# Performance work log

Measured on AMD Instinct MI355X. Metric: run time of the kernel, lower is better.

The kernel has to match this reference:

```python
import jax, jax.numpy as jnp
import numpy as np

NEG_SLOPE = 0.2


def setup_inputs() -> dict:
    key = jax.random.key(0)
    ks = jax.random.split(key, 6)
    N, E, IN, H, D = 50000, 800000, 256, 4, 64
    x = jax.random.normal(ks[0], (N, IN), dtype=jnp.float32)
    edge_index = jax.random.randint(ks[1], (2, E), 0, N, dtype=jnp.int64)
    W = jax.random.normal(ks[2], (IN, H * D), dtype=jnp.float32) / np.sqrt(IN)
    att_src = jax.random.normal(ks[3], (H, D), dtype=jnp.float32) / np.sqrt(D)
    att_dst = jax.random.normal(ks[4], (H, D), dtype=jnp.float32) / np.sqrt(D)
    bias = jnp.zeros((H * D,), dtype=jnp.float32)
    return {"x": x, "edge_index": edge_index, "W": W,
            "att_src": att_src, "att_dst": att_dst, "bias": bias}


def reference(x, edge_index, W, att_src, att_dst, bias):
    N = x.shape[0]
    H, D = att_src.shape
    # add self-loops (PyG GATConv default add_self_loops=True)
    loops = jnp.arange(N, dtype=edge_index.dtype)
    src = jnp.concatenate([edge_index[0], loops])  # [E']
    dst = jnp.concatenate([edge_index[1], loops])  # [E']
    # per-head linear transform: [N, H, D]
    h = (x @ W).reshape(N, H, D)
    # per-node attention logits per head: [N, H]
    a_s = jnp.einsum('nhd,hd->nh', h, att_src)
    a_d = jnp.einsum('nhd,hd->nh', h, att_dst)
    # per-edge raw attention: [E', H]
    e = jax.nn.leaky_relu(a_s[src] + a_d[dst], NEG_SLOPE)
    # softmax over edges grouped by destination node (stable)
    m = jax.ops.segment_max(e, dst, num_segments=N)
    e = jnp.exp(e - m[dst])
    s = jax.ops.segment_sum(e, dst, num_segments=N)
    alpha = e / s[dst]  # every node has a self-loop -> s > 0
    # weighted scatter-aggregate: [N, H, D]
    out = jax.ops.segment_sum(alpha[:, :, None] * h[src], dst, num_segments=N)
    # concat heads + bias; dropout=0.0 -> identity
    return out.reshape(N, H * D) + bias
```

## Files before the change

### kernel.cpp

```cpp
#include <hip/hip_runtime.h>
#include <hip/hip_bf16.h>

#define NEG_SLOPE 0.2f
#define HPAD 264

typedef short short8 __attribute__((ext_vector_type(8)));
typedef float floatx4 __attribute__((ext_vector_type(4)));
typedef unsigned short ushort8v __attribute__((ext_vector_type(8)));
typedef unsigned short ushort4v __attribute__((ext_vector_type(4)));
typedef unsigned int uint4v __attribute__((ext_vector_type(4)));

__device__ __forceinline__ float bf2f_raw(unsigned short u) {
    union { float f; unsigned u; } c; c.u = ((unsigned)u) << 16; return c.f;
}
__device__ __forceinline__ float asf(unsigned u) {
    union { float f; unsigned u; } c; c.u = u; return c.f;
}
__device__ __forceinline__ unsigned short f2bf_raw(float f) {
    union { float f; unsigned u; } c; c.f = f;
    unsigned u = c.u;
    u += 0x7FFFu + ((u >> 16) & 1u);
    return (unsigned short)(u >> 16);
}
__device__ __forceinline__ float ldf(const void* p, size_t i, int f32) {
    return f32 ? ((const float*)p)[i] : bf2f_raw(((const unsigned short*)p)[i]);
}
__device__ __forceinline__ unsigned short ldbf(const void* p, size_t i, int f32) {
    return f32 ? f2bf_raw(((const float*)p)[i]) : ((const unsigned short*)p)[i];
}
__device__ __forceinline__ int clampN(long long v, int N) {
    if (v < 0) v = 0;
    if (v >= N) v = N - 1;
    return (int)v;
}
__device__ __forceinline__ float lrelu(float v) { return v > 0.f ? v : NEG_SLOPE * v; }

__global__ __launch_bounds__(256) void detect_kernel(
    const unsigned short* __restrict__ x, const unsigned short* __restrict__ W,
    const unsigned short* __restrict__ as_, const unsigned short* __restrict__ ad_,
    const unsigned* __restrict__ edge_w, int* __restrict__ flags, int edge_words)
{
    __shared__ float sm[256];
    __shared__ unsigned su[256];
    const int t = threadIdx.x;

    float mx = 0.f, mw = 0.f, ma = 0.f;
    for (int i = t; i < 4096; i += 256) {
        float v = fabsf(bf2f_raw(x[i]));
        mx = fmaxf(mx, (v == v && v < 3e38f) ? v : 1e9f);
    }
    for (int i = t; i < 4096; i += 256) {
        float v = fabsf(bf2f_raw(W[i]));
        mw = fmaxf(mw, (v == v && v < 3e38f) ? v : 1e9f);
    }
    {
        float v1 = fabsf(bf2f_raw(as_[t]));
        float v2 = fabsf(bf2f_raw(ad_[t]));
        v1 = (v1 == v1 && v1 < 3e38f) ? v1 : 1e9f;
        v2 = (v2 == v2 && v2 < 3e38f) ? v2 : 1e9f;
        ma = fmaxf(v1, v2);
    }
    unsigned ow = 0;
    {
        int i = 2 * t + 1;
        if (i < edge_words) ow = edge_w[i];
    }

    sm[t] = mx; __syncthreads();
    for (int s = 128; s; s >>= 1) { if (t < s) sm[t] = fmaxf(sm[t], sm[t + s]); __syncthreads(); }
    if (t == 0) flags[0] = sm[0] > 100.f;
    __syncthreads();

    sm[t] = mw; __syncthreads();
    for (int s = 128; s; s >>= 1) { if (t < s) sm[t] = fmaxf(sm[t], sm[t + s]); __syncthreads(); }
    if (t == 0) flags[1] = sm[0] > 100.f;
    __syncthreads();

    sm[t] = ma; __syncthreads();
    for (int s = 128; s; s >>= 1) { if (t < s) sm[t] = fmaxf(sm[t], sm[t + s]); __syncthreads(); }
    if (t == 0) flags[2] = sm[0] > 100.f;
    __syncthreads();

    su[t] = ow; __syncthreads();
    for (int s = 128; s; s >>= 1) { if (t < s) su[t] |= su[t + s]; __syncthreads(); }
    if (t == 0) flags[3] = (su[0] == 0u);
}

__global__ __launch_bounds__(256) void wt_kernel(
    const void* __restrict__ W, unsigned short* __restrict__ Wt,
    const int* __restrict__ flags, int* __restrict__ deg8, int* __restrict__ bsync, int N8)
{
    int i = blockIdx.x * 256 + threadIdx.x;
    #pragma unroll
    for (int j = 0; j < 7; ++j) {
        int z = i + j * 65536;
        if (z < N8) deg8[z] = 0;
    }
    if (i < 256) bsync[i] = 0;
    int j = i & 7;
    int l = (i >> 3) & 63;
    int ks = (i >> 9) & 7;
    int c = i >> 12;
    int k = ks * 32 + (l >> 4) * 8 + j;
    int n = c * 16 + (l & 15);
    Wt[i] = ldbf(W, (size_t)k * 256 + n, flags[1]);
}

__global__ __launch_bounds__(256) void count_kernel(
    const void* __restrict__ edge, int* __restrict__ deg8, int* __restrict__ rank,
    const int* __restrict__ flags, int E, int N)
{
    const int base = (blockIdx.x * 256 + threadIdx.x) * 4;
    if (base >= E) return;
    int* my = deg8 + (size_t)(blockIdx.x & 7) * N;
    const int cnt = (E - base < 4) ? (E - base) : 4;
    int d[4];
    if (flags[3]) {
        const long long* p = (const long long*)edge + E + base;
        #pragma unroll
        for (int k = 0; k < 4; ++k) d[k] = clampN((k < cnt) ? p[k] : 0, N);
    } else {
        const int* p = (const int*)edge + E + base;
        #pragma unroll
        for (int k = 0; k < 4; ++k) d[k] = clampN((k < cnt) ? (long long)p[k] : 0, N);
    }
    int r[4] = {0, 0, 0, 0};
    #pragma unroll
    for (int k = 0; k < 4; ++k)
        if (k < cnt) r[k] = atomicAdd(&my[d[k]], 1);
    #pragma unroll
    for (int k = 0; k < 4; ++k)
        if (k < cnt) rank[base + k] = r[k];
}

__global__ __launch_bounds__(512) void gemm_kernel(
    const void* __restrict__ x, const unsigned short* __restrict__ Wt,
    const void* __restrict__ att_src, const void* __restrict__ att_dst,
    unsigned short* __restrict__ h_out, float* __restrict__ a_s, float* __restrict__ a_d,
    const int* __restrict__ flags, int N, int ntiles, int gemm_blocks)
{
    __shared__ unsigned short sh_h[32][HPAD];
    __shared__ float sh_a[2][32][4];

    const int w = threadIdx.x >> 6;
    const int head = w >> 1;
    const int st = w & 1;
    const int l = threadIdx.x & 63;
    const int lane16 = l & 15;
    const int quad = l >> 4;
    const int xf = flags[0], af = flags[2];
    const int n0w = head * 64;

    float as_att[4], ad_att[4];
    #pragma unroll
    for (int nt = 0; nt < 4; ++nt) {
        as_att[nt] = ldf(att_src, n0w + nt * 16 + lane16, af);
        ad_att[nt] = ldf(att_dst, n0w + nt * 16 + lane16, af);
    }

    for (int tile = blockIdx.x; tile < ntiles; tile += gemm_blocks) {
        const int m0 = tile * 32;
        int r0 = m0 + st * 16 + lane16;
        if (r0 >= N) r0 = N - 1;

        floatx4 acc[4];
        #pragma unroll
        for (int nt = 0; nt < 4; ++nt) acc[nt] = (floatx4){0.f, 0.f, 0.f, 0.f};

        const unsigned short* wp0 = Wt + (((size_t)head * 32) * 64 + l) * 8;

        #pragma unroll
        for (int half = 0; half < 2; ++half) {
            short8 fa[4];
            if (!xf) {
                const char* b0 = (const char*)x + ((size_t)r0 * 256 + quad * 8) * 2 + half * 256;
                #pragma unroll
                for (int k4 = 0; k4 < 4; ++k4)
                    fa[k4] = *(const short8*)(b0 + k4 * 64);
            } else {
                const float* b0 = (const float*)x + (size_t)r0 * 256 + quad * 8 + half * 128;
                #pragma unroll
                for (int k4 = 0; k4 < 4; ++k4) {
                    #pragma unroll
                    for (int j = 0; j < 8; ++j)
                        fa[k4][j] = (short)f2bf_raw(b0[k4 * 32 + j]);
                }
            }

            #pragma unroll
            for (int k4 = 0; k4 < 4; ++k4) {
                const unsigned short* wp = wp0 + (size_t)(half * 4 + k4) * 512;
                #pragma unroll
                for (int nt = 0; nt < 4; ++nt) {
                    short8 fb = *(const short8*)(wp + nt * 4096);
                    acc[nt] = __builtin_amdgcn_mfma_f32_16x16x32_bf16(fa[k4], fb, acc[nt], 0, 0, 0);
                }
            }
        }

        __syncthreads();

        #pragma unroll
        for (int nt = 0; nt < 4; ++nt) {
            #pragma unroll
            for (int r = 0; r < 4; ++r) {
                sh_h[st * 16 + quad * 4 + r][n0w + nt * 16 + lane16] = f2bf_raw(acc[nt][r]);
            }
        }
        #pragma unroll
        for (int r = 0; r < 4; ++r) {
            float vs = acc[0][r] * as_att[0] + acc[1][r] * as_att[1]
                     + acc[2][r] * as_att[2] + acc[3][r] * as_att[3];
            float vd = acc[0][r] * ad_att[0] + acc[1][r] * ad_att[1]
                     + acc[2][r] * ad_att[2] + acc[3][r] * ad_att[3];
            vs += __shfl_xor(vs, 1); vs += __shfl_xor(vs, 2);
            vs += __shfl_xor(vs, 4); vs += __shfl_xor(vs, 8);
            vd += __shfl_xor(vd, 1); vd += __shfl_xor(vd, 2);
            vd += __shfl_xor(vd, 4); vd += __shfl_xor(vd, 8);
            if (lane16 == 0) {
                const int row = st * 16 + quad * 4 + r;
                sh_a[0][row][head] = vs;
                sh_a[1][row][head] = vd;
            }
        }

        __syncthreads();

        #pragma unroll
        for (int p = 0; p < 2; ++p) {
            const int c = p * 512 + threadIdx.x;
            const int row = c >> 5;
            const int ch = c & 31;
            if (m0 + row < N) {
                ushort8v v = *(const ushort8v*)&sh_h[row][ch * 8];
                *(ushort8v*)(h_out + (size_t)(m0 + row) * 256 + ch * 8) = v;
            }
        }
        {
            const int t = threadIdx.x;
            if (t < 32) {
                if (m0 + t < N)
                    *(floatx4*)&a_s[(size_t)(m0 + t) * 4] = *(const floatx4*)&sh_a[0][t][0];
            } else if (t >= 64 && t < 96) {
                const int r = t - 64;
                if (m0 + r < N)
                    *(floatx4*)&a_d[(size_t)(m0 + r) * 4] = *(const floatx4*)&sh_a[1][r][0];
            }
        }
    }
}

__global__ __launch_bounds__(256) void scan_fused_kernel(
    const int* __restrict__ deg8, int* __restrict__ deg,
    int* __restrict__ row_off, int* __restrict__ cursor8,
    int* __restrict__ bsum, int* __restrict__ bbase, int* __restrict__ bsync,
    int N, int nb)
{
    __shared__ int sh[256];
    __shared__ int is_last;
    __shared__ int sbase;
    const int b = blockIdx.x, t = threadIdx.x;
    const int base_i = b * 1024 + t * 4;
    int v[4], ts = 0;
    #pragma unroll
    for (int i = 0; i < 4; ++i) {
        int idx = base_i + i;
        int tot = 0;
        if (idx < N) {
            #pragma unroll
            for (int x = 0; x < 8; ++x) tot += deg8[(size_t)x * N + idx];
        }
        v[i] = tot;
        ts += tot;
    }
    sh[t] = ts; __syncthreads();
    for (int off = 1; off < 256; off <<= 1) {
        int add = (t >= off) ? sh[t - off] : 0;
        __syncthreads();
        sh[t] += add;
        __syncthreads();
    }
    if (t == 255) {
        __hip_atomic_store(&bsum[b], sh[255], __ATOMIC_RELEASE, __HIP_MEMORY_SCOPE_AGENT);
        int arrived = __hip_atomic_fetch_add(&bsync[0], 1, __ATOMIC_ACQ_REL, __HIP_MEMORY_SCOPE_AGENT);
        is_last = (arrived == nb - 1);
    }
    __syncthreads();
    if (is_last) {
        if (nb <= 64) {
            if (t < 64) {
                int val = (t < nb)
                    ? __hip_atomic_load(&bsum[t], __ATOMIC_ACQUIRE, __HIP_MEMORY_SCOPE_AGENT) : 0;
                int incl = val;
                #pragma unroll
                for (int off = 1; off < 64; off <<= 1) {
                    int u = __shfl_up(incl, off);
                    if (t >= off) incl += u;
                }
                if (t < nb)
                    __hip_atomic_store(&bbase[t], incl - val, __ATOMIC_RELEASE, __HIP_MEMORY_SCOPE_AGENT);
            }
        } else if (t == 0) {
            int run = 0;
            for (int i = 0; i < nb; ++i) {
                int s = __hip_atomic_load(&bsum[i], __ATOMIC_ACQUIRE, __HIP_MEMORY_SCOPE_AGENT);
                __hip_atomic_store(&bbase[i], run, __ATOMIC_RELEASE, __HIP_MEMORY_SCOPE_AGENT);
                run += s;
            }
        }
        __syncthreads();
        if (t == 0)
            __hip_atomic_store(&bsync[1], 1, __ATOMIC_RELEASE, __HIP_MEMORY_SCOPE_AGENT);
    }
    if (t == 0) {
        while (__hip_atomic_load(&bsync[1], __ATOMIC_ACQUIRE, __HIP_MEMORY_SCOPE_AGENT) == 0) {}
        sbase = __hip_atomic_load(&bbase[b], __ATOMIC_RELAXED, __HIP_MEMORY_SCOPE_AGENT);
    }
    __syncthreads();
    int run = sbase + sh[t] - ts;
    #pragma unroll
    for (int i = 0; i < 4; ++i) {
        int idx = base_i + i;
        if (idx < N) {
            row_off[idx] = run;
            deg[idx] = v[i];
            int c = run;
            #pragma unroll
            for (int x = 0; x < 8; ++x) {
                cursor8[(size_t)x * N + idx] = c;
                c += deg8[(size_t)x * N + idx];
            }
        }
        run += v[i];
    }
}

__global__ __launch_bounds__(256) void scatter_kernel(
    const void* __restrict__ edge, const int* __restrict__ cursor8,
    const int* __restrict__ rank, int* __restrict__ elist,
    const int* __restrict__ flags, int E, int N)
{
    const int base = (blockIdx.x * 256 + threadIdx.x) * 4;
    if (base >= E) return;
    const int* mybase = cursor8 + (size_t)(blockIdx.x & 7) * N;
    const int cnt = (E - base < 4) ? (E - base) : 4;
    int s[4], d[4];
    if (flags[3]) {
        const long long* ps = (const long long*)edge + base;
        const long long* pd = (const long long*)edge + E + base;
        #pragma unroll
        for (int k = 0; k < 4; ++k) {
            s[k] = clampN((k < cnt) ? ps[k] : 0, N);
            d[k] = clampN((k < cnt) ? pd[k] : 0, N);
        }
    } else {
        const int* ps = (const int*)edge + base;
        const int* pd = (const int*)edge + E + base;
        #pragma unroll
        for (int k = 0; k < 4; ++k) {
            s[k] = clampN((k < cnt) ? (long long)ps[k] : 0, N);
            d[k] = clampN((k < cnt) ? (long long)pd[k] : 0, N);
        }
    }
    #pragma unroll
    for (int k = 0; k < 4; ++k) {
        if (k < cnt) {
            int pos = mybase[d[k]] + rank[base + k];
            elist[pos] = s[k];
        }
    }
}

__global__ __launch_bounds__(256) void aggregate_kernel(
    const int* __restrict__ row_off, const int* __restrict__ deg,
    const int* __restrict__ elist,
    const float* __restrict__ a_s, const float* __restrict__ a_d,
    const unsigned short* __restrict__ h_ws,
    const void* __restrict__ bias, void* __restrict__ out,
    const int* __restrict__ flags, int N)
{
    const int n = blockIdx.x * 4 + (threadIdx.x >> 6);
    if (n >= N) return;
    const int lane = threadIdx.x & 63;
    const int q = lane >> 4;
    const int li = lane & 15;
    const int head = li >> 2;
    const int col0 = li * 16;

    const int dn = deg[n];
    const int row = row_off[n];
    const float adn = a_d[n * 4 + head];
    const float self_logit = lrelu(a_s[n * 4 + head] + adn);

    float acc[16];
    {
        const uint4v* hp = (const uint4v*)(h_ws + (size_t)n * 256 + col0);
        uint4v ha = hp[0], hb = hp[1];
        #pragma unroll
        for (int w = 0; w < 4; ++w) {
            acc[2 * w]         = (q == 0) ? asf(ha[w] << 16) : 0.f;
            acc[2 * w + 1]     = (q == 0) ? asf(ha[w] & 0xffff0000u) : 0.f;
            acc[8 + 2 * w]     = (q == 0) ? asf(hb[w] << 16) : 0.f;
            acc[8 + 2 * w + 1] = (q == 0) ? asf(hb[w] & 0xffff0000u) : 0.f;
        }
    }
    float ssum = (q == 0) ? 1.f : 0.f;

    float asA, asB;
    uint4v hA0, hA1, hB0, hB1;
    int sC, sD;
    {
        int e0 = q, e1 = 4 + q, e2 = 8 + q, e3 = 12 + q;
        int s0 = (e0 < dn) ? elist[row + e0] : n;
        int s1 = (e1 < dn) ? elist[row + e1] : n;
        sC = (e2 < dn) ? elist[row + e2] : n;
        sD = (e3 < dn) ? elist[row + e3] : n;
        asA = a_s[s0 * 4 + head];
        asB = a_s[s1 * 4 + head];
        const uint4v* pA = (const uint4v*)(h_ws + (size_t)s0 * 256 + col0);
        const uint4v* pB = (const uint4v*)(h_ws + (size_t)s1 * 256 + col0);
        hA0 = pA[0]; hA1 = pA[1];
        hB0 = pB[0]; hB1 = pB[1];
    }

    for (int c0 = 0; c0 < dn; c0 += 8) {
        {
            float p = __expf(lrelu(asA + adn) - self_logit);
            p = (c0 + q < dn) ? p : 0.f;
            ssum += p;
            #pragma unroll
            for (int w = 0; w < 4; ++w) {
                acc[2 * w]         += p * asf(hA0[w] << 16);
                acc[2 * w + 1]     += p * asf(hA0[w] & 0xffff0000u);
                acc[8 + 2 * w]     += p * asf(hA1[w] << 16);
                acc[8 + 2 * w + 1] += p * asf(hA1[w] & 0xffff0000u);
            }
        }
        {
            asA = a_s[sC * 4 + head];
            const uint4v* p = (const uint4v*)(h_ws + (size_t)sC * 256 + col0);
            hA0 = p[0]; hA1 = p[1];
            int e = c0 + 16 + q;
            sC = (e < dn) ? elist[row + e] : n;
        }
        {
            float p = __expf(lrelu(asB + adn) - self_logit);
            p = (c0 + 4 + q < dn) ? p : 0.f;
            ssum += p;
            #pragma unroll
            for (int w = 0; w < 4; ++w) {
                acc[2 * w]         += p * asf(hB0[w] << 16);
                acc[2 * w + 1]     += p * asf(hB0[w] & 0xffff0000u);
                acc[8 + 2 * w]     += p * asf(hB1[w] << 16);
                acc[8 + 2 * w + 1] += p * asf(hB1[w] & 0xffff0000u);
            }
        }
        {
            asB = a_s[sD * 4 + head];
            const uint4v* p = (const uint4v*)(h_ws + (size_t)sD * 256 + col0);
            hB0 = p[0]; hB1 = p[1];
            int e = c0 + 20 + q;
            sD = (e < dn) ? elist[row + e] : n;
        }
    }

    #pragma unroll
    for (int j = 0; j < 16; ++j) {
        acc[j] += __shfl_xor(acc[j], 16);
        acc[j] += __shfl_xor(acc[j], 32);
    }
    float stot = ssum + __shfl_xor(ssum, 16);
    stot += __shfl_xor(stot, 32);

    const float inv = 1.f / stot;
    const int j0 = q * 4;
    const int bf32 = flags[2];
    float o[4];
    #pragma unroll
    for (int k = 0; k < 4; ++k)
        o[k] = acc[j0 + k] * inv + ldf(bias, col0 + j0 + k, bf32);
    if (flags[0]) {
        float* op = (float*)out + (size_t)n * 256 + col0 + j0;
        __builtin_nontemporal_store((floatx4){o[0], o[1], o[2], o[3]}, (floatx4*)op);
    } else {
        ushort4v ov;
        #pragma unroll
        for (int k = 0; k < 4; ++k) ov[k] = f2bf_raw(o[k]);
        __builtin_nontemporal_store(ov,
            (ushort4v*)((unsigned short*)out + (size_t)n * 256 + col0 + j0));
    }
}

__global__ __launch_bounds__(256) void sentinel_kernel(unsigned short* out, size_t n, float v) {
    size_t i = (size_t)blockIdx.x * 256 + threadIdx.x;
    if (i < n) out[i] = f2bf_raw(v);
}

extern "C" void kernel_launch(void* const* d_in, const int* in_sizes, int n_in,
                              void* d_out, int out_size, void* d_ws, size_t ws_size,
                              hipStream_t stream) {
    const void* x       = d_in[0];
    const void* edge    = d_in[1];
    const void* W       = d_in[2];
    const void* att_src = d_in[3];
    const void* att_dst = d_in[4];
    const void* bias    = d_in[5];

    const int N = in_sizes[0] / 256;
    const int E = in_sizes[1] / 2;

    char* ws = (char*)d_ws;
    size_t off = 256;
    int*   flags   = (int*)ws;
    float* a_s     = (float*)(ws + off); off += (size_t)N * 4 * sizeof(float);
    float* a_d     = (float*)(ws + off); off += (size_t)N * 4 * sizeof(float);
    int*   deg     = (int*)(ws + off);   off += (size_t)N * sizeof(int);
    int*   row_off = (int*)(ws + off);   off += (size_t)N * sizeof(int);
    int*   bsum    = (int*)(ws + off);   off += 256 * sizeof(int);
    int*   bbase   = (int*)(ws + off);   off += 256 * sizeof(int);
    int*   bsync   = (int*)(ws + off);   off += 256 * sizeof(int);
    unsigned short* Wt = (unsigned short*)(ws + off); off += 65536 * sizeof(unsigned short);
    size_t elist_bytes = (size_t)E * sizeof(int);
    size_t deg8_bytes  = (size_t)8 * N * sizeof(int);
    int*   elist   = (int*)(ws + off);
    int*   deg8    = (int*)(ws + off);   off += (elist_bytes > deg8_bytes ? elist_bytes : deg8_bytes);
    int*   cursor8 = (int*)(ws + off);   off += deg8_bytes;
    int*   rank    = (int*)(ws + off);   off += (size_t)E * sizeof(int);
    unsigned short* h_ws = (unsigned short*)(ws + off);
    const size_t need = off + (size_t)N * 256 * sizeof(unsigned short);

    if (ws_size < need) {
        float v = (float)(ws_size >> 20) * 1000.0f;
        size_t n = (size_t)out_size;
        sentinel_kernel<<<(unsigned)((n + 255) / 256), 256, 0, stream>>>(
            (unsigned short*)d_out, n, v);
        return;
    }

    int edge_words = (2 * E < 512) ? 2 * E : 512;
    detect_kernel<<<1, 256, 0, stream>>>(
        (const unsigned short*)x, (const unsigned short*)W,
        (const unsigned short*)att_src, (const unsigned short*)att_dst,
        (const unsigned*)edge, flags, edge_words);

    wt_kernel<<<256, 256, 0, stream>>>(W, Wt, flags, deg8, bsync, 8 * N);

    const int edge_blocks = (E + 1023) / 1024;
    count_kernel<<<edge_blocks, 256, 0, stream>>>(edge, deg8, rank, flags, E, N);

    const int ntiles = (N + 31) / 32;
    const int gemm_blocks = 1024;
    gemm_kernel<<<gemm_blocks, 512, 0, stream>>>(
        x, Wt, att_src, att_dst, h_ws, a_s, a_d, flags, N, ntiles, gemm_blocks);

    const int nb = (N + 1023) / 1024;
    scan_fused_kernel<<<nb, 256, 0, stream>>>(
        deg8, deg, row_off, cursor8, bsum, bbase, bsync, N, nb);

    scatter_kernel<<<edge_blocks, 256, 0, stream>>>(edge, cursor8, rank, elist, flags, E, N);

    aggregate_kernel<<<(N + 3) / 4, 256, 0, stream>>>(
        row_off, deg, elist, a_s, a_d, h_ws, bias, d_out, flags, N);
}
```

Measured before the change: 282.1 us.

## Fuse degree counting into GEMM launch and make aggregation persistent

Merges the edge degree-count pass into the GEMM kernel by interleaving count blocks among GEMM blocks in a single launch, so the atomic counting overlaps with the matrix multiply and one launch is saved. Scatter and count now use 512-thread blocks covering 2048 edges each. The aggregate kernel becomes a grid-stride persistent loop over nodes with a fixed 2048-block grid. The trade-off is that count blocks now carry the GEMM kernel's large shared-memory and register footprint, which may reduce occupancy, and the persistent loop may balance work worse across nodes of uneven degree.

```diff
diff --git a/kernel.cpp b/kernel.cpp
--- a/kernel.cpp
+++ b/kernel.cpp
@@ -106,39 +106,46 @@
     Wt[i] = ldbf(W, (size_t)k * 256 + n, flags[1]);
 }
 
-__global__ __launch_bounds__(256) void count_kernel(
-    const void* __restrict__ edge, int* __restrict__ deg8, int* __restrict__ rank,
-    const int* __restrict__ flags, int E, int N)
-{
-    const int base = (blockIdx.x * 256 + threadIdx.x) * 4;
-    if (base >= E) return;
-    int* my = deg8 + (size_t)(blockIdx.x & 7) * N;
-    const int cnt = (E - base < 4) ? (E - base) : 4;
-    int d[4];
-    if (flags[3]) {
-        const long long* p = (const long long*)edge + E + base;
-        #pragma unroll
-        for (int k = 0; k < 4; ++k) d[k] = clampN((k < cnt) ? p[k] : 0, N);
-    } else {
-        const int* p = (const int*)edge + E + base;
-        #pragma unroll
-        for (int k = 0; k < 4; ++k) d[k] = clampN((k < cnt) ? (long long)p[k] : 0, N);
-    }
-    int r[4] = {0, 0, 0, 0};
-    #pragma unroll
-    for (int k = 0; k < 4; ++k)
-        if (k < cnt) r[k] = atomicAdd(&my[d[k]], 1);
-    #pragma unroll
-    for (int k = 0; k < 4; ++k)
-        if (k < cnt) rank[base + k] = r[k];
-}
-
-__global__ __launch_bounds__(512) void gemm_kernel(
+__global__ __launch_bounds__(512) void gemm_count_kernel(
     const void* __restrict__ x, const unsigned short* __restrict__ Wt,
     const void* __restrict__ att_src, const void* __restrict__ att_dst,
     unsigned short* __restrict__ h_out, float* __restrict__ a_s, float* __restrict__ a_d,
-    const int* __restrict__ flags, int N, int ntiles, int gemm_blocks)
+    const void* __restrict__ edge, int* __restrict__ deg8, int* __restrict__ rank,
+    const int* __restrict__ flags, int N, int E, int ntiles,
+    int ngemm, int ncount, int ntotal)
 {
+    const unsigned long long bi = blockIdx.x;
+    const unsigned before = (unsigned)((bi * (unsigned long long)ncount) / ntotal);
+    const unsigned after  = (unsigned)(((bi + 1) * (unsigned long long)ncount) / ntotal);
+
+    if (after != before) {
+        const int cb = (int)before;
+        const int base = cb * 2048 + threadIdx.x * 4;
+        if (base >= E) return;
+        int* my = deg8 + (size_t)(cb & 7) * N;
+        const int cnt = (E - base < 4) ? (E - base) : 4;
+        int d[4];
+        if (flags[3]) {
+            const long long* p = (const long long*)edge + E + base;
+            #pragma unroll
+            for (int k = 0; k < 4; ++k) d[k] = clampN((k < cnt) ? p[k] : 0, N);
+        } else {
+            const int* p = (const int*)edge + E + base;
+            #pragma unroll
+            for (int k = 0; k < 4; ++k) d[k] = clampN((k < cnt) ? (long long)p[k] : 0, N);
+        }
+        int r[4] = {0, 0, 0, 0};
+        #pragma unroll
+        for (int k = 0; k < 4; ++k)
+            if (k < cnt) r[k] = atomicAdd(&my[d[k]], 1);
+        #pragma unroll
+        for (int k = 0; k < 4; ++k)
+            if (k < cnt) rank[base + k] = r[k];
+        return;
+    }
+
+    const int gb = (int)(bi - before);
+
     __shared__ unsigned short sh_h[32][HPAD];
     __shared__ float sh_a[2][32][4];
 
@@ -158,7 +165,7 @@
         ad_att[nt] = ldf(att_dst, n0w + nt * 16 + lane16, af);
     }
 
-    for (int tile = blockIdx.x; tile < ntiles; tile += gemm_blocks) {
+    for (int tile = gb; tile < ntiles; tile += ngemm) {
         const int m0 = tile * 32;
         int r0 = m0 + st * 16 + lane16;
         if (r0 >= N) r0 = N - 1;
@@ -335,12 +342,12 @@
     }
 }
 
-__global__ __launch_bounds__(256) void scatter_kernel(
+__global__ __launch_bounds__(512) void scatter_kernel(
     const void* __restrict__ edge, const int* __restrict__ cursor8,
     const int* __restrict__ rank, int* __restrict__ elist,
     const int* __restrict__ flags, int E, int N)
 {
-    const int base = (blockIdx.x * 256 + threadIdx.x) * 4;
+    const int base = blockIdx.x * 2048 + threadIdx.x * 4;
     if (base >= E) return;
     const int* mybase = cursor8 + (size_t)(blockIdx.x & 7) * N;
     const int cnt = (E - base < 4) ? (E - base) : 4;
@@ -377,117 +384,119 @@
     const float* __restrict__ a_s, const float* __restrict__ a_d,
     const unsigned short* __restrict__ h_ws,
     const void* __restrict__ bias, void* __restrict__ out,
-    const int* __restrict__ flags, int N)
+    const int* __restrict__ flags, int N, int nwaves)
 {
-    const int n = blockIdx.x * 4 + (threadIdx.x >> 6);
-    if (n >= N) return;
+    const int gw = blockIdx.x * 4 + (threadIdx.x >> 6);
     const int lane = threadIdx.x & 63;
     const int q = lane >> 4;
     const int li = lane & 15;
     const int head = li >> 2;
     const int col0 = li * 16;
-
-    const int dn = deg[n];
-    const int row = row_off[n];
-    const float adn = a_d[n * 4 + head];
-    const float self_logit = lrelu(a_s[n * 4 + head] + adn);
-
-    float acc[16];
-    {
-        const uint4v* hp = (const uint4v*)(h_ws + (size_t)n * 256 + col0);
-        uint4v ha = hp[0], hb = hp[1];
-        #pragma unroll
-        for (int w = 0; w < 4; ++w) {
-            acc[2 * w]         = (q == 0) ? asf(ha[w] << 16) : 0.f;
-            acc[2 * w + 1]     = (q == 0) ? asf(ha[w] & 0xffff0000u) : 0.f;
-            acc[8 + 2 * w]     = (q == 0) ? asf(hb[w] << 16) : 0.f;
-            acc[8 + 2 * w + 1] = (q == 0) ? asf(hb[w] & 0xffff0000u) : 0.f;
-        }
-    }
-    float ssum = (q == 0) ? 1.f : 0.f;
-
-    float asA, asB;
-    uint4v hA0, hA1, hB0, hB1;
-    int sC, sD;
-    {
-        int e0 = q, e1 = 4 + q, e2 = 8 + q, e3 = 12 + q;
-        int s0 = (e0 < dn) ? elist[row + e0] : n;
-        int s1 = (e1 < dn) ? elist[row + e1] : n;
-        sC = (e2 < dn) ? elist[row + e2] : n;
-        sD = (e3 < dn) ? elist[row + e3] : n;
-        asA = a_s[s0 * 4 + head];
-        asB = a_s[s1 * 4 + head];
-        const uint4v* pA = (const uint4v*)(h_ws + (size_t)s0 * 256 + col0);
-        const uint4v* pB = (const uint4v*)(h_ws + (size_t)s1 * 256 + col0);
-        hA0 = pA[0]; hA1 = pA[1];
-        hB0 = pB[0]; hB1 = pB[1];
-    }
-
-    for (int c0 = 0; c0 < dn; c0 += 8) {
+    const int bf32 = flags[2];
+    const int of32 = flags[0];
+
+    for (int n = gw; n < N; n += nwaves) {
+        const int dn = deg[n];
+        const int row = row_off[n];
+        const float adn = a_d[n * 4 + head];
+        const float self_logit = lrelu(a_s[n * 4 + head] + adn);
+
+        float acc[16];
         {
-            float p = __expf(lrelu(asA + adn) - self_logit);
-            p = (c0 + q < dn) ? p : 0.f;
-            ssum += p;
+            const uint4v* hp = (const uint4v*)(h_ws + (size_t)n * 256 + col0);
+            uint4v ha = hp[0], hb = hp[1];
             #pragma unroll
             for (int w = 0; w < 4; ++w) {
-                acc[2 * w]         += p * asf(hA0[w] << 16);
-                acc[2 * w + 1]     += p * asf(hA0[w] & 0xffff0000u);
-                acc[8 + 2 * w]     += p * asf(hA1[w] << 16);
-                acc[8 + 2 * w + 1] += p * asf(hA1[w] & 0xffff0000u);
-            }
-        }
+                acc[2 * w]         = (q == 0) ? asf(ha[w] << 16) : 0.f;
+                acc[2 * w + 1]     = (q == 0) ? asf(ha[w] & 0xffff0000u) : 0.f;
+                acc[8 + 2 * w]     = (q == 0) ? asf(hb[w] << 16) : 0.f;
+                acc[8 + 2 * w + 1] = (q == 0) ? asf(hb[w] & 0xffff0000u) : 0.f;
+            }
+        }
+        float ssum = (q == 0) ? 1.f : 0.f;
+
+        float asA, asB;
+        uint4v hA0, hA1, hB0, hB1;
+        int sC, sD;
         {
-            asA = a_s[sC * 4 + head];
-            const uint4v* p = (const uint4v*)(h_ws + (size_t)sC * 256 + col0);
-            hA0 = p[0]; hA1 = p[1];
-            int e = c0 + 16 + q;
-            sC = (e < dn) ? elist[row + e] : n;
-        }
-        {
-            float p = __expf(lrelu(asB + adn) - self_logit);
-            p = (c0 + 4 + q < dn) ? p : 0.f;
-            ssum += p;
-            #pragma unroll
-            for (int w = 0; w < 4; ++w) {
-                acc[2 * w]         += p * asf(hB0[w] << 16);
-                acc[2 * w + 1]     += p * asf(hB0[w] & 0xffff0000u);
-                acc[8 + 2 * w]     += p * asf(hB1[w] << 16);
-                acc[8 + 2 * w + 1] += p * asf(hB1[w] & 0xffff0000u);
-            }
-        }
-        {
-            asB = a_s[sD * 4 + head];
-            const uint4v* p = (const uint4v*)(h_ws + (size_t)sD * 256 + col0);
-            hB0 = p[0]; hB1 = p[1];
-            int e = c0 + 20 + q;
-            sD = (e < dn) ? elist[row + e] : n;
-        }
-    }
-
-    #pragma unroll
-    for (int j = 0; j < 16; ++j) {
-        acc[j] += __shfl_xor(acc[j], 16);
-        acc[j] += __shfl_xor(acc[j], 32);
-    }
-    float stot = ssum + __shfl_xor(ssum, 16);
-    stot += __shfl_xor(stot, 32);
-
-    const float inv = 1.f / stot;
-    const int j0 = q * 4;
-    const int bf32 = flags[2];
-    float o[4];
-    #pragma unroll
-    for (int k = 0; k < 4; ++k)
-        o[k] = acc[j0 + k] * inv + ldf(bias, col0 + j0 + k, bf32);
-    if (flags[0]) {
-        float* op = (float*)out + (size_t)n * 256 + col0 + j0;
-        __builtin_nontemporal_store((floatx4){o[0], o[1], o[2], o[3]}, (floatx4*)op);
-    } else {
-        ushort4v ov;
-        #pragma unroll
-        for (int k = 0; k < 4; ++k) ov[k] = f2bf_raw(o[k]);
-        __builtin_nontemporal_store(ov,
-            (ushort4v*)((unsigned short*)out + (size_t)n * 256 + col0 + j0));
+            int e0 = q, e1 = 4 + q, e2 = 8 + q, e3 = 12 + q;
+            int s0 = (e0 < dn) ? elist[row + e0] : n;
+            int s1 = (e1 < dn) ? elist[row + e1] : n;
+            sC = (e2 < dn) ? elist[row + e2] : n;
+            sD = (e3 < dn) ? elist[row + e3] : n;
+            asA = a_s[s0 * 4 + head];
+            asB = a_s[s1 * 4 + head];
+            const uint4v* pA = (const uint4v*)(h_ws + (size_t)s0 * 256 + col0);
+            const uint4v* pB = (const uint4v*)(h_ws + (size_t)s1 * 256 + col0);
+            hA0 = pA[0]; hA1 = pA[1];
+            hB0 = pB[0]; hB1 = pB[1];
+        }
+
+        for (int c0 = 0; c0 < dn; c0 += 8) {
+            {
+                float p = __expf(lrelu(asA + adn) - self_logit);
+                p = (c0 + q < dn) ? p : 0.f;
+                ssum += p;
+                #pragma unroll
+                for (int w = 0; w < 4; ++w) {
+                    acc[2 * w]         += p * asf(hA0[w] << 16);
+                    acc[2 * w + 1]     += p * asf(hA0[w] & 0xffff0000u);
+                    acc[8 + 2 * w]     += p * asf(hA1[w] << 16);
+                    acc[8 + 2 * w + 1] += p * asf(hA1[w] & 0xffff0000u);
+                }
+            }
+            {
+                asA = a_s[sC * 4 + head];
+                const uint4v* p = (const uint4v*)(h_ws + (size_t)sC * 256 + col0);
+                hA0 = p[0]; hA1 = p[1];
+                int e = c0 + 16 + q;
+                sC = (e < dn) ? elist[row + e] : n;
+            }
+            {
+                float p = __expf(lrelu(asB + adn) - self_logit);
+                p = (c0 + 4 + q < dn) ? p : 0.f;
+                ssum += p;
+                #pragma unroll
+                for (int w = 0; w < 4; ++w) {
+                    acc[2 * w]         += p * asf(hB0[w] << 16);
+                    acc[2 * w + 1]     += p * asf(hB0[w] & 0xffff0000u);
+                    acc[8 + 2 * w]     += p * asf(hB1[w] << 16);
+                    acc[8 + 2 * w + 1] += p * asf(hB1[w] & 0xffff0000u);
+                }
+            }
+            {
+                asB = a_s[sD * 4 + head];
+                const uint4v* p = (const uint4v*)(h_ws + (size_t)sD * 256 + col0);
+                hB0 = p[0]; hB1 = p[1];
+                int e = c0 + 20 + q;
+                sD = (e < dn) ? elist[row + e] : n;
+            }
+        }
+
+        #pragma unroll
+        for (int j = 0; j < 16; ++j) {
+            acc[j] += __shfl_xor(acc[j], 16);
+            acc[j] += __shfl_xor(acc[j], 32);
+        }
+        float stot = ssum + __shfl_xor(ssum, 16);
+        stot += __shfl_xor(stot, 32);
+
+        const float inv = 1.f / stot;
+        const int j0 = q * 4;
+        float o[4];
+        #pragma unroll
+        for (int k = 0; k < 4; ++k)
+            o[k] = acc[j0 + k] * inv + ldf(bias, col0 + j0 + k, bf32);
+        if (of32) {
+            float* op = (float*)out + (size_t)n * 256 + col0 + j0;
+            __builtin_nontemporal_store((floatx4){o[0], o[1], o[2], o[3]}, (floatx4*)op);
+        } else {
+            ushort4v ov;
+            #pragma unroll
+            for (int k = 0; k < 4; ++k) ov[k] = f2bf_raw(o[k]);
+            __builtin_nontemporal_store(ov,
+                (ushort4v*)((unsigned short*)out + (size_t)n * 256 + col0 + j0));
+        }
     }
 }
 
@@ -545,20 +554,21 @@
 
     wt_kernel<<<256, 256, 0, stream>>>(W, Wt, flags, deg8, bsync, 8 * N);
 
-    const int edge_blocks = (E + 1023) / 1024;
-    count_kernel<<<edge_blocks, 256, 0, stream>>>(edge, deg8, rank, flags, E, N);
-
     const int ntiles = (N + 31) / 32;
-    const int gemm_blocks = 1024;
-    gemm_kernel<<<gemm_blocks, 512, 0, stream>>>(
-        x, Wt, att_src, att_dst, h_ws, a_s, a_d, flags, N, ntiles, gemm_blocks);
+    const int ngemm = 1024;
+    const int ncount = (E + 2047) / 2048;
+    const int ntotal = ngemm + ncount;
+    gemm_count_kernel<<<ntotal, 512, 0, stream>>>(
+        x, Wt, att_src, att_dst, h_ws, a_s, a_d, edge, deg8, rank,
+        flags, N, E, ntiles, ngemm, ncount, ntotal);
 
     const int nb = (N + 1023) / 1024;
     scan_fused_kernel<<<nb, 256, 0, stream>>>(
         deg8, deg, row_off, cursor8, bsum, bbase, bsync, N, nb);
 
-    scatter_kernel<<<edge_blocks, 256, 0, stream>>>(edge, cursor8, rank, elist, flags, E, N);
-
-    aggregate_kernel<<<(N + 3) / 4, 256, 0, stream>>>(
-        row_off, deg, elist, a_s, a_d, h_ws, bias, d_out, flags, N);
-}
+    scatter_kernel<<<ncount, 512, 0, stream>>>(edge, cursor8, rank, elist, flags, E, N);
+
+    const int agg_blocks = 2048;
+    aggregate_kernel<<<agg_blocks, 256, 0, stream>>>(
+        row_off, deg, elist, a_s, a_d, h_ws, bias, d_out, flags, N, agg_blocks * 4);
+}
```

Measured after the change: 263.7 us. 1.07x faster.
